# Optimization experiments

Measured on AMD Instinct MI355X. Metric: run time of the kernel, lower is better.

Reference implementation:

```python
import math
import jax, jax.numpy as jnp
import numpy as np

B, N, CS, CZ, CH, H, PQ, PV = 1, 4096, 512, 128, 64, 16, 4, 8
BQ, BK = 32, 128
NB = N // BQ
CZ4 = CZ // 4
INF = 100000.0
EPS = 1e-8


def quat_to_rot(q):
    w, x, y, z = q[..., 0], q[..., 1], q[..., 2], q[..., 3]
    return jnp.stack([
        jnp.stack([1 - 2 * (y * y + z * z), 2 * (x * y - w * z), 2 * (x * z + w * y)], -1),
        jnp.stack([2 * (x * y + w * z), 1 - 2 * (x * x + z * z), 2 * (y * z - w * x)], -1),
        jnp.stack([2 * (x * z - w * y), 2 * (y * z + w * x), 1 - 2 * (x * x + y * y)], -1),
    ], -2)


def setup_inputs() -> dict:
    key = jax.random.key(0)
    ks = jax.random.split(key, 16)
    s = jax.random.normal(ks[0], (B, N, CS), jnp.float32)
    z = jax.random.normal(ks[1], (B, NB, BQ, BK, CZ), jnp.float32)
    trans = jax.random.normal(ks[2], (B, N, 3), jnp.float32) * 10.0
    quat = jax.random.normal(ks[3], (B, N, 4), jnp.float32)
    quat = quat / jnp.linalg.norm(quat, axis=-1, keepdims=True)
    rots = quat_to_rot(quat)
    s_mask = jnp.ones((B, N), jnp.float32)
    pad = (BK - BQ) // 2  # key window centered on each query block
    key_idx = (jnp.arange(NB)[:, None] * BQ - pad + jnp.arange(BK)[None, :]).astype(jnp.int32)

    def w(k, shp):
        return jax.random.normal(k, shp, jnp.float32) * (1.0 / math.sqrt(shp[0]))

    return {
        's': s, 'z': z, 'trans': trans, 'rots': rots, 's_mask': s_mask, 'key_idx': key_idx,
        'Wq': w(ks[4], (CS, H * CH)), 'Wk': w(ks[5], (CS, H * CH)), 'Wv': w(ks[6], (CS, H * CH)),
        'Wqp': w(ks[7], (CS, H * PQ * 3)), 'Wkvp': w(ks[8], (CS, H * (PQ + PV) * 3)),
        'Wb': w(ks[9], (CZ, H)), 'Wdz': w(ks[10], (CZ, CZ4)),
        'head_weights': jnp.full((H,), float(np.log(np.e - 1.0)), jnp.float32),  # softplus^-1(1)
        'Wout': w(ks[11], (H * (CZ4 + CH + PV * 4), CS)),
        'g_s': jnp.ones((CS,), jnp.float32), 'b_s': jnp.zeros((CS,), jnp.float32),
        'g_z': jnp.ones((CZ,), jnp.float32), 'b_z': jnp.zeros((CZ,), jnp.float32),
    }


def _ln(x, g, b):
    m = jnp.mean(x, -1, keepdims=True)
    v = jnp.mean((x - m) ** 2, -1, keepdims=True)
    return (x - m) * jax.lax.rsqrt(v + 1e-5) * g + b


def _ipa(s, z, trans, rots, s_mask, key_idx, Wq, Wk, Wv, Wqp, Wkvp, Wb, Wdz,
         head_weights, Wout, g_s, b_s, g_z, b_z):
    s_n = _ln(s, g_s, b_s)
    z_n = _ln(z, g_z, b_z)

    valid = (key_idx >= 0) & (key_idx < N)            # [NB, BK]
    idx = jnp.clip(key_idx, 0, N - 1)
    vf = valid.astype(s.dtype)[None]                  # [1, NB, BK]

    def gk(x):  # gather key window: [B,N,...] -> [B,NB,BK,...]
        return x[:, idx]

    sq = s_n.reshape(B, NB, BQ, CS)
    sk = gk(s_n) * vf[..., None]                      # zero-pad out-of-range keys

    tq = trans.reshape(B, NB, BQ, 3)
    rq = rots.reshape(B, NB, BQ, 3, 3)
    tk = gk(trans) * vf[..., None]
    rk = jnp.where(valid[None, :, :, None, None], gk(rots), jnp.eye(3, dtype=rots.dtype))

    q = (sq @ Wq).reshape(B, NB, BQ, H, CH)
    k = (sk @ Wk).reshape(B, NB, BK, H, CH)
    v = (sk @ Wv).reshape(B, NB, BK, H, CH)

    q_pts = (sq @ Wqp).reshape(B, NB, BQ, H * PQ, 3)
    q_pts = jnp.einsum('bnqij,bnqpj->bnqpi', rq, q_pts) + tq[:, :, :, None, :]
    q_pts = q_pts.reshape(B, NB, BQ, H, PQ, 3)

    kv_pts = (sk @ Wkvp).reshape(B, NB, BK, H * (PQ + PV), 3)
    kv_pts = jnp.einsum('bnkij,bnkpj->bnkpi', rk, kv_pts) + tk[:, :, :, None, :]
    kv_pts = kv_pts.reshape(B, NB, BK, H, PQ + PV, 3)
    k_pts, v_pts = kv_pts[..., :PQ, :], kv_pts[..., PQ:, :]

    bias = jnp.einsum('bnqkc,ch->bnqkh', z_n, Wb)
    a = jnp.einsum('bnqhc,bnkhc->bnqkh', q, k) * math.sqrt(1.0 / (3 * CH))
    a = a + math.sqrt(1.0 / 3) * bias

    disp = q_pts[:, :, :, None] - k_pts[:, :, None]   # [B,NB,BQ,BK,H,PQ,3]
    pt_att = jnp.sum(disp ** 2, -1)                   # [B,NB,BQ,BK,H,PQ]
    hw = jax.nn.softplus(head_weights) * math.sqrt(1.0 / (3 * (PQ * 9.0 / 2)))
    pt_att = -0.5 * jnp.sum(pt_att * hw[:, None], -1)  # [B,NB,BQ,BK,H]

    qm = s_mask.reshape(B, NB, BQ)
    km = gk(s_mask) * vf
    amask = INF * (qm[:, :, :, None] * km[:, :, None, :] - 1.0)

    a = a + pt_att + amask[..., None]
    a = jax.nn.softmax(jnp.swapaxes(a, -1, -2), axis=-1)  # [B,NB,BQ,H,BK]

    o = jnp.einsum('bnqhk,bnkhc->bnqhc', a, v).reshape(B, NB, BQ, H * CH)

    o_pt = jnp.einsum('bnqhk,bnkhpc->bnqhpc', a, v_pts)
    o_pt = jnp.einsum('bnqji,bnqhpj->bnqhpi', rq, o_pt - tq[:, :, :, None, None, :])
    o_pt_norm = jnp.sqrt(jnp.sum(o_pt ** 2, -1) + EPS).reshape(B, NB, BQ, H * PV)
    o_pt = o_pt.reshape(B, NB, BQ, H * PV * 3)

    pair_z = z_n @ Wdz                                # [B,NB,BQ,BK,CZ4]
    o_pair = jnp.einsum('bnqhk,bnqkc->bnqhc', a, pair_z).reshape(B, NB, BQ, H * CZ4)

    out = jnp.concatenate([o, o_pt, o_pt_norm, o_pair], -1) @ Wout
    return out.reshape(B, N, CS)


def reference(s, z, trans, rots, s_mask, key_idx, Wq, Wk, Wv, Wqp, Wkvp, Wb, Wdz,
              head_weights, Wout, g_s, b_s, g_z, b_z):
    return _ipa(s, z, trans, rots, s_mask, key_idx, Wq, Wk, Wv, Wqp, Wkvp, Wb, Wdz,
                head_weights, Wout, g_s, b_s, g_z, b_z)
```

## Files before the change

### kernel.cpp

```cpp
#include <hip/hip_runtime.h>
#include <math.h>

#define D_N 4096
#define PBW 3072
#define PPW 768
#define OFFK 1024
#define OFFV 2048
#define CATW 2048

typedef __bf16 bf16_t;
typedef __bf16 bf16x8 __attribute__((ext_vector_type(8)));
typedef __bf16 bf16x4 __attribute__((ext_vector_type(4)));
typedef float f32x4 __attribute__((ext_vector_type(4)));

__device__ __forceinline__ void gld16(const void* g, void* l) {
    __builtin_amdgcn_global_load_lds((const __attribute__((address_space(1))) unsigned int*)g,
                                     (__attribute__((address_space(3))) unsigned int*)l, 16, 0, 0);
}

__global__ __launch_bounds__(256) void k_prep(
    const float* __restrict__ Wq, const float* __restrict__ Wk, const float* __restrict__ Wv,
    const float* __restrict__ Wqp, const float* __restrict__ Wkvp, const float* __restrict__ Wout,
    const float* __restrict__ Wb, const float* __restrict__ Wdz,
    const float* __restrict__ gz, const float* __restrict__ bz,
    const float* __restrict__ s, const float* __restrict__ g_s, const float* __restrict__ b_s,
    bf16_t* __restrict__ wcatT, bf16_t* __restrict__ WoutT,
    bf16_t* __restrict__ WzT, float* __restrict__ Kv, bf16_t* __restrict__ s_nb)
{
    __shared__ float T[64][65];
    const int bx = blockIdx.x;
    const int tid = threadIdx.x;
    if (bx < 736) {
        const float* src; int ld, coff, r0;
        bf16_t* dst; int Rdst;
        if (bx < 480) {
            int c0 = (bx % 60) * 64;
            r0 = (bx / 60) * 64;
            if (c0 < 1024)      { src = Wq;   ld = 1024; coff = c0; }
            else if (c0 < 2048) { src = Wk;   ld = 1024; coff = c0 - 1024; }
            else if (c0 < 3072) { src = Wv;   ld = 1024; coff = c0 - 2048; }
            else if (c0 < 3264) { src = Wqp;  ld = 192;  coff = c0 - 3072; }
            else                { src = Wkvp; ld = 576;  coff = c0 - 3264; }
            dst = wcatT + (size_t)c0 * 512; Rdst = 512;
        } else {
            int b = bx - 480;
            int c0 = (b & 7) * 64;
            r0 = (b >> 3) * 64;
            src = Wout; ld = 512; coff = c0;
            dst = WoutT + (size_t)c0 * 2048; Rdst = 2048;
        }
        {
            int rr = tid >> 2, cb = (tid & 3) * 16;
            const float* p = src + (size_t)(r0 + rr) * ld + coff + cb;
            #pragma unroll
            for (int i = 0; i < 4; ++i)
                *(float4*)&T[rr][cb + i * 4] = *(const float4*)(p + i * 4);
        }
        __syncthreads();
        {
            int cc = tid >> 2, rb = (tid & 3) * 16;
            bf16_t* o = dst + (size_t)cc * Rdst + r0 + rb;
            bf16x8 o0, o1;
            #pragma unroll
            for (int j = 0; j < 8; ++j) o0[j] = (bf16_t)T[rb + j][cc];
            #pragma unroll
            for (int j = 0; j < 8; ++j) o1[j] = (bf16_t)T[rb + 8 + j][cc];
            *(bf16x8*)(o) = o0;
            *(bf16x8*)(o + 8) = o1;
        }
    } else if (bx == 736) {
        for (int i = tid; i < 6144; i += 256) {
            int j = i >> 7, c = i & 127;
            float w = (j < 16) ? Wb[c * 16 + j] : Wdz[c * 32 + (j - 16)];
            WzT[i] = (bf16_t)(gz[c] * w);
        }
        if (tid < 48) {
            int j = tid;
            float acc = 0.f;
            for (int c = 0; c < 128; ++c) {
                float w = (j < 16) ? Wb[c * 16 + j] : Wdz[c * 32 + (j - 16)];
                acc += bz[c] * w;
            }
            Kv[j] = acc;
        }
    } else {
        int row = (bx - 737) * 4 + (tid >> 6);
        int lane = tid & 63;
        const float4* p = (const float4*)(s + (size_t)row * 512);
        float4 v0 = p[lane];
        float4 v1 = p[lane + 64];
        float sum = v0.x + v0.y + v0.z + v0.w + v1.x + v1.y + v1.z + v1.w;
        float sq  = v0.x*v0.x + v0.y*v0.y + v0.z*v0.z + v0.w*v0.w
                  + v1.x*v1.x + v1.y*v1.y + v1.z*v1.z + v1.w*v1.w;
        #pragma unroll
        for (int off = 1; off < 64; off <<= 1) {
            sum += __shfl_xor(sum, off);
            sq  += __shfl_xor(sq, off);
        }
        float m = sum * (1.0f / 512.0f);
        float var = sq * (1.0f / 512.0f) - m * m;
        float rs = rsqrtf(var + 1e-5f);
        int c = lane * 4;
        int c2 = 256 + lane * 4;
        bf16x4 r0, r1;
        r0[0] = (bf16_t)((v0.x - m) * rs * g_s[c+0] + b_s[c+0]);
        r0[1] = (bf16_t)((v0.y - m) * rs * g_s[c+1] + b_s[c+1]);
        r0[2] = (bf16_t)((v0.z - m) * rs * g_s[c+2] + b_s[c+2]);
        r0[3] = (bf16_t)((v0.w - m) * rs * g_s[c+3] + b_s[c+3]);
        r1[0] = (bf16_t)((v1.x - m) * rs * g_s[c2+0] + b_s[c2+0]);
        r1[1] = (bf16_t)((v1.y - m) * rs * g_s[c2+1] + b_s[c2+1]);
        r1[2] = (bf16_t)((v1.z - m) * rs * g_s[c2+2] + b_s[c2+2]);
        r1[3] = (bf16_t)((v1.w - m) * rs * g_s[c2+3] + b_s[c2+3]);
        *(bf16x4*)(s_nb + (size_t)row * 512 + c)  = r0;
        *(bf16x4*)(s_nb + (size_t)row * 512 + c2) = r1;
    }
}

__global__ __launch_bounds__(256) void gemm_proj(const bf16_t* __restrict__ A, const bf16_t* __restrict__ BT,
    bf16_t* __restrict__ projb, float* __restrict__ projp)
{
    __shared__ bf16_t Asl[128][32];
    __shared__ bf16_t Bsl[128][32];
    const int tid = threadIdx.x, lane = tid & 63, w = tid >> 6;
    const int row0 = blockIdx.y * 128, col0 = blockIdx.x * 128;
    const int wr = (w >> 1) * 64, wc = (w & 1) * 64;
    const int K = 512;
    const int sr = lane >> 2, k8 = (lane & 3) * 8;
    const bf16_t* Ab = A + (size_t)(row0 + w * 32 + sr) * K + k8;
    const bf16_t* Bb = BT + (size_t)(col0 + w * 32 + sr) * K + k8;
    f32x4 acc[4][4];
    #pragma unroll
    for (int m = 0; m < 4; ++m)
        #pragma unroll
        for (int n = 0; n < 4; ++n) acc[m][n] = (f32x4){0.f,0.f,0.f,0.f};
    for (int k0 = 0; k0 < K; k0 += 32) {
        __syncthreads();
        gld16(Ab + k0,          &Asl[w * 32][0]);
        gld16(Ab + k0 + 16 * K, &Asl[w * 32 + 16][0]);
        gld16(Bb + k0,          &Bsl[w * 32][0]);
        gld16(Bb + k0 + 16 * K, &Bsl[w * 32 + 16][0]);
        __syncthreads();
        bf16x8 af[4], bfr[4];
        #pragma unroll
        for (int m = 0; m < 4; ++m) af[m]  = *(const bf16x8*)&Asl[wr + m*16 + (lane & 15)][(lane >> 4) * 8];
        #pragma unroll
        for (int n = 0; n < 4; ++n) bfr[n] = *(const bf16x8*)&Bsl[wc + n*16 + (lane & 15)][(lane >> 4) * 8];
        #pragma unroll
        for (int m = 0; m < 4; ++m)
            #pragma unroll
            for (int n = 0; n < 4; ++n)
                acc[m][n] = __builtin_amdgcn_mfma_f32_16x16x32_bf16(af[m], bfr[n], acc[m][n], 0, 0, 0);
    }
    if (col0 < 3072) {
        #pragma unroll
        for (int m = 0; m < 4; ++m)
            #pragma unroll
            for (int n = 0; n < 4; ++n)
                #pragma unroll
                for (int i = 0; i < 4; ++i)
                    projb[(size_t)(row0 + wr + m*16 + (lane >> 4)*4 + i) * PBW + col0 + wc + n*16 + (lane & 15)]
                        = (bf16_t)acc[m][n][i];
    } else {
        #pragma unroll
        for (int m = 0; m < 4; ++m)
            #pragma unroll
            for (int n = 0; n < 4; ++n)
                #pragma unroll
                for (int i = 0; i < 4; ++i)
                    projp[(size_t)(row0 + wr + m*16 + (lane >> 4)*4 + i) * PPW + col0 - 3072 + wc + n*16 + (lane & 15)]
                        = acc[m][n][i];
    }
}

__global__ __launch_bounds__(256) void k_zbias4(const float* __restrict__ z,
    const bf16_t* __restrict__ WzT, const float* __restrict__ Kv,
    float* __restrict__ biasT, bf16_t* __restrict__ pzT)
{
    __shared__ __align__(16) float zbuf[2][64][128];
    const int tid = threadIdx.x, lane = tid & 63, w = tid >> 6;
    const int r16 = lane & 15, kg = lane >> 4;
    bf16x8 bfz[3][4];
    #pragma unroll
    for (int nt = 0; nt < 3; ++nt)
        #pragma unroll
        for (int kc = 0; kc < 4; ++kc)
            bfz[nt][kc] = *(const bf16x8*)(WzT + (size_t)(nt * 16 + r16) * 128 + kc * 32 + kg * 8);
    float K0 = Kv[r16], K1 = Kv[16 + r16], K2 = Kv[32 + r16];
    asm volatile("s_waitcnt vmcnt(0)" ::: "memory");
    __builtin_amdgcn_sched_barrier(0);

    const int gid = blockIdx.x * 4 + w;
    const char* zb = (const char*)z + (size_t)gid * 64 * 512;
    char* lb0 = (char*)&zbuf[0][w * 16][0];
    char* lb1 = (char*)&zbuf[1][w * 16][0];

#define STAGE(i, lb) { \
    const char* gp_ = zb + (size_t)(i) * 8192 + lane * 16; \
    _Pragma("unroll") \
    for (int c_ = 0; c_ < 8; ++c_) gld16(gp_ + c_ * 1024, (lb) + c_ * 1024); }

#define PROCESS(i, b) { \
    const float* rp = &zbuf[b][w * 16 + r16][kg * 8]; \
    float4 za[4], zc[4]; \
    float sum = 0.f, sq = 0.f; \
    _Pragma("unroll") \
    for (int kc = 0; kc < 4; ++kc) { \
        float4 a_ = *(const float4*)(rp + kc * 32); \
        float4 b_ = *(const float4*)(rp + kc * 32 + 4); \
        za[kc] = a_; zc[kc] = b_; \
        sum += a_.x + a_.y + a_.z + a_.w + b_.x + b_.y + b_.z + b_.w; \
        sq  += a_.x*a_.x + a_.y*a_.y + a_.z*a_.z + a_.w*a_.w + b_.x*b_.x + b_.y*b_.y + b_.z*b_.z + b_.w*b_.w; \
    } \
    sum += __shfl_xor(sum, 16); sq += __shfl_xor(sq, 16); \
    sum += __shfl_xor(sum, 32); sq += __shfl_xor(sq, 32); \
    float m_ = sum * (1.0f / 128.0f); \
    float rs_ = rsqrtf(sq * (1.0f / 128.0f) - m_ * m_ + 1e-5f); \
    bf16x8 af[4]; \
    _Pragma("unroll") \
    for (int kc = 0; kc < 4; ++kc) { \
        af[kc][0] = (bf16_t)((za[kc].x - m_) * rs_); \
        af[kc][1] = (bf16_t)((za[kc].y - m_) * rs_); \
        af[kc][2] = (bf16_t)((za[kc].z - m_) * rs_); \
        af[kc][3] = (bf16_t)((za[kc].w - m_) * rs_); \
        af[kc][4] = (bf16_t)((zc[kc].x - m_) * rs_); \
        af[kc][5] = (bf16_t)((zc[kc].y - m_) * rs_); \
        af[kc][6] = (bf16_t)((zc[kc].z - m_) * rs_); \
        af[kc][7] = (bf16_t)((zc[kc].w - m_) * rs_); \
    } \
    f32x4 acc0 = (f32x4){0.f,0.f,0.f,0.f}; \
    f32x4 acc1 = (f32x4){0.f,0.f,0.f,0.f}; \
    f32x4 acc2 = (f32x4){0.f,0.f,0.f,0.f}; \
    _Pragma("unroll") \
    for (int kc = 0; kc < 4; ++kc) { \
        acc0 = __builtin_amdgcn_mfma_f32_16x16x32_bf16(af[kc], bfz[0][kc], acc0, 0, 0, 0); \
        acc1 = __builtin_amdgcn_mfma_f32_16x16x32_bf16(af[kc], bfz[1][kc], acc1, 0, 0, 0); \
        acc2 = __builtin_amdgcn_mfma_f32_16x16x32_bf16(af[kc], bfz[2][kc], acc2, 0, 0, 0); \
    } \
    const int t_ = gid * 4 + (i); \
    const int rowq_ = t_ >> 3; \
    const int k0_ = ((t_ & 7) << 4) + kg * 4; \
    float4 bw = {acc0[0] + K0, acc0[1] + K0, acc0[2] + K0, acc0[3] + K0}; \
    *(float4*)&biasT[((size_t)rowq_ * 16 + r16) * 128 + k0_] = bw; \
    bf16x4 p1, p2; \
    _Pragma("unroll") \
    for (int i2 = 0; i2 < 4; ++i2) { p1[i2] = (bf16_t)(acc1[i2] + K1); p2[i2] = (bf16_t)(acc2[i2] + K2); } \
    *(bf16x4*)&pzT[((size_t)rowq_ * 32 + r16) * 128 + k0_] = p1; \
    *(bf16x4*)&pzT[((size_t)rowq_ * 32 + 16 + r16) * 128 + k0_] = p2; }

#define LDS_DRAIN asm volatile("s_waitcnt lgkmcnt(0)" ::: "memory"); __builtin_amdgcn_sched_barrier(0);

    STAGE(0, lb0);
    STAGE(1, lb1);
    asm volatile("s_waitcnt vmcnt(8)" ::: "memory");
    __builtin_amdgcn_sched_barrier(0);
    PROCESS(0, 0);
    LDS_DRAIN
    STAGE(2, lb0);
    asm volatile("s_waitcnt vmcnt(8)" ::: "memory");
    __builtin_amdgcn_sched_barrier(0);
    PROCESS(1, 1);
    LDS_DRAIN
    STAGE(3, lb1);
    asm volatile("s_waitcnt vmcnt(8)" ::: "memory");
    __builtin_amdgcn_sched_barrier(0);
    PROCESS(2, 0);
    asm volatile("s_waitcnt vmcnt(0)" ::: "memory");
    __builtin_amdgcn_sched_barrier(0);
    PROCESS(3, 1);
#undef STAGE
#undef PROCESS
#undef LDS_DRAIN
}

__global__ __launch_bounds__(256) void k_attn4(
    const bf16_t* __restrict__ projb, const float* __restrict__ projp,
    const float* __restrict__ biasT, const float* __restrict__ rots,
    const float* __restrict__ trans, const float* __restrict__ smask,
    const int* __restrict__ kidx, const float* __restrict__ hwraw,
    bf16_t* __restrict__ catb, bf16_t* __restrict__ Pbf)
{
    __shared__ __align__(16) char pool[51840];
    bf16_t (*Qs)[72]   = (bf16_t(*)[72])pool;
    bf16_t (*Ks)[72]   = (bf16_t(*)[72])(pool + 32 * 72 * 2);
    bf16_t (*Vt)[136]  = (bf16_t(*)[136])pool;
    float  (*att)[132] = (float(*)[132])(pool + 26112);
    bf16_t (*Ps)[136]  = (bf16_t(*)[136])(pool + 26112);
    float  (*optmp)[33]= (float(*)[33])(pool + 26112 + 8704);
    float  (*kp_s)[12] = (float(*)[12])(pool + 43008);
    float  (*qp_s)[12] = (float(*)[12])(pool + 49152);
    float*  km_s       = (float*)(pool + 50688);
    float*  qm_s       = (float*)(pool + 51200);
    int*    rows_s     = (int*)(pool + 51328);

    const int wgid = blockIdx.x;
    const int swz = (wgid & 7) * 256 + (wgid >> 3);
    const int h = swz >> 7;
    const int nblk = swz & 127;
    const int tid = threadIdx.x;
    const int lane = tid & 63;
    const int w = tid >> 6;
    const int rowq0 = nblk * 32;
    const float hw = log1pf(__expf(hwraw[h])) * 0.13608276348795434f;

    if (tid < 128) {
        int ki = kidx[nblk * 128 + tid];
        int valid = (ki >= 0 && ki < D_N);
        int rr = ki < 0 ? 0 : (ki > D_N - 1 ? D_N - 1 : ki);
        rows_s[tid] = rr;
        km_s[tid] = valid ? smask[rr] : 0.0f;
    } else if (tid < 160) {
        qm_s[tid - 128] = smask[rowq0 + tid - 128];
    }
    __syncthreads();
    {
        int q = tid >> 3, cg = (tid & 7) * 8;
        *(bf16x8*)&Qs[q][cg] = *(const bf16x8*)(projb + (size_t)(rowq0 + q) * PBW + h * 64 + cg);
    }
    float Rk[9], tk0 = 0.f, tk1 = 0.f, tk2 = 0.f;
    if (tid < 128) {
        int rr = rows_s[tid];
        const float* Rp = rots + (size_t)rr * 9;
        const float* tp = trans + (size_t)rr * 3;
        #pragma unroll
        for (int e = 0; e < 9; ++e) Rk[e] = Rp[e];
        tk0 = tp[0]; tk1 = tp[1]; tk2 = tp[2];
        const float* kp = projp + (size_t)rr * PPW + 192 + h * 36;
        float4 p0 = *(const float4*)kp;
        float4 p1 = *(const float4*)(kp + 4);
        float4 p2 = *(const float4*)(kp + 8);
        float xs[4] = {p0.x, p0.w, p1.z, p2.y};
        float ys[4] = {p0.y, p1.x, p1.w, p2.z};
        float zs[4] = {p0.z, p1.y, p2.x, p2.w};
        #pragma unroll
        for (int p = 0; p < 4; ++p) {
            kp_s[tid][p*3+0] = Rk[0]*xs[p] + Rk[1]*ys[p] + Rk[2]*zs[p] + tk0;
            kp_s[tid][p*3+1] = Rk[3]*xs[p] + Rk[4]*ys[p] + Rk[5]*zs[p] + tk1;
            kp_s[tid][p*3+2] = Rk[6]*xs[p] + Rk[7]*ys[p] + Rk[8]*zs[p] + tk2;
        }
    } else {
        int j = tid - 128;
        {
            int q = j >> 2, p = j & 3;
            const float* Rp = rots + (size_t)(rowq0 + q) * 9;
            const float* tp = trans + (size_t)(rowq0 + q) * 3;
            const float* qp = projp + (size_t)(rowq0 + q) * PPW + h * 12 + p * 3;
            float x = qp[0], y = qp[1], zc = qp[2];
            qp_s[q][p*3+0] = Rp[0]*x + Rp[1]*y + Rp[2]*zc + tp[0];
            qp_s[q][p*3+1] = Rp[3]*x + Rp[4]*y + Rp[5]*zc + tp[1];
            qp_s[q][p*3+2] = Rp[6]*x + Rp[7]*y + Rp[8]*zc + tp[2];
        }
        {
            const bf16_t* pK = projb + (size_t)rows_s[j] * PBW + OFFK + h * 64;
            #pragma unroll
            for (int u = 0; u < 8; ++u)
                *(bf16x8*)&Ks[j][u * 8] = *(const bf16x8*)(pK + u * 8);
        }
    }
    __syncthreads();
    {
        #pragma unroll
        for (int j = 0; j < 4; ++j) {
            int T = w * 4 + j;
            int m = T & 1, n = T >> 1;
            f32x4 acc = (f32x4){0.f,0.f,0.f,0.f};
            #pragma unroll
            for (int kc = 0; kc < 2; ++kc) {
                bf16x8 a = *(const bf16x8*)&Qs[m*16 + (lane & 15)][kc*32 + (lane >> 4) * 8];
                bf16x8 b = *(const bf16x8*)&Ks[n*16 + (lane & 15)][kc*32 + (lane >> 4) * 8];
                acc = __builtin_amdgcn_mfma_f32_16x16x32_bf16(a, b, acc, 0, 0, 0);
            }
            #pragma unroll
            for (int i = 0; i < 4; ++i)
                att[m*16 + (lane >> 4)*4 + i][n*16 + (lane & 15)] = acc[i];
        }
    }
    __syncthreads();
    if (tid < 128) {
        const float* vp = projp + (size_t)rows_s[tid] * PPW + 192 + h * 36 + 12;
        float4 a0 = *(const float4*)(vp);
        float4 a1 = *(const float4*)(vp + 4);
        float4 a2 = *(const float4*)(vp + 8);
        float4 a3 = *(const float4*)(vp + 12);
        float4 a4 = *(const float4*)(vp + 16);
        float4 a5 = *(const float4*)(vp + 20);
        float xs[8] = {a0.x, a0.w, a1.z, a2.y, a3.x, a3.w, a4.z, a5.y};
        float ys[8] = {a0.y, a1.x, a1.w, a2.z, a3.y, a4.x, a4.w, a5.z};
        float zs[8] = {a0.z, a1.y, a2.x, a2.w, a3.z, a4.y, a5.x, a5.w};
        #pragma unroll
        for (int p = 0; p < 8; ++p) {
            Vt[64 + p*3 + 0][tid] = (bf16_t)(Rk[0]*xs[p] + Rk[1]*ys[p] + Rk[2]*zs[p] + tk0);
            Vt[64 + p*3 + 1][tid] = (bf16_t)(Rk[3]*xs[p] + Rk[4]*ys[p] + Rk[5]*zs[p] + tk1);
            Vt[64 + p*3 + 2][tid] = (bf16_t)(Rk[6]*xs[p] + Rk[7]*ys[p] + Rk[8]*zs[p] + tk2);
        }
        {
            bf16x8 zz = {};
            *(bf16x8*)&Vt[88 + (tid & 7)][(tid >> 3) * 8] = zz;
        }
    } else {
        int krow = tid - 128;
        const bf16_t* p = projb + (size_t)rows_s[krow] * PBW + OFFV + h * 64;
        #pragma unroll
        for (int u4 = 0; u4 < 8; ++u4) {
            bf16x8 v = *(const bf16x8*)(p + u4 * 8);
            #pragma unroll
            for (int jj = 0; jj < 8; ++jj) Vt[u4 * 8 + jj][krow] = v[jj];
        }
    }
    {
        int q = tid >> 3, kg = tid & 7;
        float qp[12];
        #pragma unroll
        for (int e = 0; e < 12; ++e) qp[e] = qp_s[q][e];
        float qm = qm_s[q];
        const float* bT = biasT + ((size_t)(rowq0 + q) * 16 + h) * 128;
        #pragma unroll
        for (int j2 = 0; j2 < 16; ++j2) {
            int k = kg + j2 * 8;
            float4 k0 = *(const float4*)&kp_s[k][0];
            float4 k1 = *(const float4*)&kp_s[k][4];
            float4 k2 = *(const float4*)&kp_s[k][8];
            float d0 = qp[0]-k0.x, d1 = qp[1]-k0.y, d2_ = qp[2]-k0.z, d3 = qp[3]-k0.w;
            float d4 = qp[4]-k1.x, d5 = qp[5]-k1.y, d6 = qp[6]-k1.z, d7 = qp[7]-k1.w;
            float d8 = qp[8]-k2.x, d9 = qp[9]-k2.y, d10 = qp[10]-k2.z, d11 = qp[11]-k2.w;
            float dd = d0*d0+d1*d1+d2_*d2_+d3*d3+d4*d4+d5*d5+d6*d6+d7*d7+d8*d8+d9*d9+d10*d10+d11*d11;
            float val = att[q][k] * 0.07216878364870323f
                      + 0.5773502691896258f * bT[k]
                      + 100000.0f * (qm * km_s[k] - 1.0f)
                      - 0.5f * hw * dd;
            att[q][k] = val;
        }
    }
    __syncthreads();
    {
        int q = tid >> 3, kg = tid & 7;
        float l[16];
        #pragma unroll
        for (int j2 = 0; j2 < 16; ++j2) l[j2] = att[q][kg + j2 * 8];
        float mx = l[0];
        #pragma unroll
        for (int j2 = 1; j2 < 16; ++j2) mx = fmaxf(mx, l[j2]);
        mx = fmaxf(mx, __shfl_xor(mx, 1));
        mx = fmaxf(mx, __shfl_xor(mx, 2));
        mx = fmaxf(mx, __shfl_xor(mx, 4));
        float se = 0.f;
        #pragma unroll
        for (int j2 = 0; j2 < 16; ++j2) { l[j2] = __expf(l[j2] - mx); se += l[j2]; }
        se += __shfl_xor(se, 1);
        se += __shfl_xor(se, 2);
        se += __shfl_xor(se, 4);
        float inv = 1.0f / se;
        __syncthreads();
        bf16_t* pg = Pbf + ((size_t)(rowq0 + q) * 16 + h) * 128;
        #pragma unroll
        for (int j2 = 0; j2 < 16; ++j2) {
            bf16_t pb = (bf16_t)(l[j2] * inv);
            Ps[q][kg + j2 * 8] = pb;
            pg[kg + j2 * 8] = pb;
        }
    }
    __syncthreads();
    {
        #pragma unroll
        for (int j = 0; j < 3; ++j) {
            int T = w * 3 + j;
            int m = T & 1, n = T >> 1;
            f32x4 acc = (f32x4){0.f,0.f,0.f,0.f};
            #pragma unroll
            for (int kc = 0; kc < 4; ++kc) {
                bf16x8 a = *(const bf16x8*)&Ps[m*16 + (lane & 15)][kc*32 + (lane >> 4) * 8];
                bf16x8 b = *(const bf16x8*)&Vt[n*16 + (lane & 15)][kc*32 + (lane >> 4) * 8];
                acc = __builtin_amdgcn_mfma_f32_16x16x32_bf16(a, b, acc, 0, 0, 0);
            }
            int rowb = m * 16 + (lane >> 4) * 4;
            int col = lane & 15;
            if (n < 4) {
                #pragma unroll
                for (int i = 0; i < 4; ++i)
                    catb[(size_t)(rowq0 + rowb + i) * CATW + h * 64 + n * 16 + col] = (bf16_t)acc[i];
            } else {
                #pragma unroll
                for (int i = 0; i < 4; ++i)
                    optmp[rowb + i][(n - 4) * 16 + col] = acc[i];
            }
        }
    }
    __syncthreads();
    {
        int q = tid >> 3, pp = tid & 7;
        float sx = optmp[q][pp * 3 + 0];
        float sy = optmp[q][pp * 3 + 1];
        float sz = optmp[q][pp * 3 + 2];
        const float* R = rots + (size_t)(rowq0 + q) * 9;
        const float* t = trans + (size_t)(rowq0 + q) * 3;
        float x = sx - t[0], y = sy - t[1], z2 = sz - t[2];
        float ox = R[0] * x + R[3] * y + R[6] * z2;
        float oy = R[1] * x + R[4] * y + R[7] * z2;
        float oz = R[2] * x + R[5] * y + R[8] * z2;
        bf16_t* cp = catb + (size_t)(rowq0 + q) * CATW;
        cp[1024 + h * 24 + pp * 3 + 0] = (bf16_t)ox;
        cp[1024 + h * 24 + pp * 3 + 1] = (bf16_t)oy;
        cp[1024 + h * 24 + pp * 3 + 2] = (bf16_t)oz;
        cp[1408 + h * 8 + pp] = (bf16_t)sqrtf(ox * ox + oy * oy + oz * oz + 1e-8f);
    }
}

__global__ __launch_bounds__(256) void k_opair(const bf16_t* __restrict__ Pbf,
    const bf16_t* __restrict__ pzT, bf16_t* __restrict__ catb)
{
    int tid = threadIdx.x, lane = tid & 63, w = tid >> 6;
    size_t rowq = (size_t)blockIdx.x * 4 + w;
    const bf16_t* Pp = Pbf + rowq * 2048;
    const bf16_t* zp = pzT + rowq * 4096;
    bf16x8 pa[4];
    #pragma unroll
    for (int kc = 0; kc < 4; ++kc)
        pa[kc] = *(const bf16x8*)(Pp + (size_t)(lane & 15) * 128 + kc * 32 + (lane >> 4) * 8);
    #pragma unroll
    for (int ct = 0; ct < 2; ++ct) {
        f32x4 acc = (f32x4){0.f,0.f,0.f,0.f};
        #pragma unroll
        for (int kc = 0; kc < 4; ++kc) {
            bf16x8 b = *(const bf16x8*)(zp + (size_t)(ct * 16 + (lane & 15)) * 128 + kc * 32 + (lane >> 4) * 8);
            acc = __builtin_amdgcn_mfma_f32_16x16x32_bf16(pa[kc], b, acc, 0, 0, 0);
        }
        #pragma unroll
        for (int i = 0; i < 4; ++i) {
            int hh = (lane >> 4) * 4 + i;
            catb[rowq * CATW + 1536 + hh * 32 + ct * 16 + (lane & 15)] = (bf16_t)acc[i];
        }
    }
}

__global__ __launch_bounds__(256) void gemm_out(const bf16_t* __restrict__ A, const bf16_t* __restrict__ BT,
    float* __restrict__ C)
{
    __shared__ bf16_t Asl[64][32];
    __shared__ bf16_t Bsl[128][32];
    const int tid = threadIdx.x, lane = tid & 63, w = tid >> 6;
    const int row0 = blockIdx.y * 64, col0 = blockIdx.x * 128;
    const int wr = (w >> 1) * 32, wc = (w & 1) * 64;
    const int K = 2048;
    const int sr = lane >> 2, k8 = (lane & 3) * 8;
    const bf16_t* Ab = A + (size_t)(row0 + w * 16 + sr) * K + k8;
    const bf16_t* Bb = BT + (size_t)(col0 + w * 32 + sr) * K + k8;
    f32x4 acc[2][4];
    #pragma unroll
    for (int m = 0; m < 2; ++m)
        #pragma unroll
        for (int n = 0; n < 4; ++n) acc[m][n] = (f32x4){0.f,0.f,0.f,0.f};
    for (int k0 = 0; k0 < K; k0 += 32) {
        __syncthreads();
        gld16(Ab + k0,          &Asl[w * 16][0]);
        gld16(Bb + k0,          &Bsl[w * 32][0]);
        gld16(Bb + k0 + 16 * K, &Bsl[w * 32 + 16][0]);
        __syncthreads();
        bf16x8 af[2], bfr[4];
        #pragma unroll
        for (int m = 0; m < 2; ++m) af[m]  = *(const bf16x8*)&Asl[wr + m*16 + (lane & 15)][(lane >> 4) * 8];
        #pragma unroll
        for (int n = 0; n < 4; ++n) bfr[n] = *(const bf16x8*)&Bsl[wc + n*16 + (lane & 15)][(lane >> 4) * 8];
        #pragma unroll
        for (int m = 0; m < 2; ++m)
            #pragma unroll
            for (int n = 0; n < 4; ++n)
                acc[m][n] = __builtin_amdgcn_mfma_f32_16x16x32_bf16(af[m], bfr[n], acc[m][n], 0, 0, 0);
    }
    #pragma unroll
    for (int m = 0; m < 2; ++m)
        #pragma unroll
        for (int n = 0; n < 4; ++n)
            #pragma unroll
            for (int i = 0; i < 4; ++i)
                C[(size_t)(row0 + wr + m*16 + (lane >> 4)*4 + i) * 512 + col0 + wc + n*16 + (lane & 15)] = acc[m][n][i];
}

extern "C" void kernel_launch(void* const* d_in, const int* in_sizes, int n_in,
                              void* d_out, int out_size, void* d_ws, size_t ws_size,
                              hipStream_t stream)
{
    (void)in_sizes; (void)n_in; (void)out_size;
    const float* s     = (const float*)d_in[0];
    const float* z     = (const float*)d_in[1];
    const float* trans = (const float*)d_in[2];
    const float* rots  = (const float*)d_in[3];
    const float* smask = (const float*)d_in[4];
    const int*   kidx  = (const int*)d_in[5];
    const float* Wq    = (const float*)d_in[6];
    const float* Wk    = (const float*)d_in[7];
    const float* Wv    = (const float*)d_in[8];
    const float* Wqp   = (const float*)d_in[9];
    const float* Wkvp  = (const float*)d_in[10];
    const float* Wb    = (const float*)d_in[11];
    const float* Wdz   = (const float*)d_in[12];
    const float* hw    = (const float*)d_in[13];
    const float* Wout  = (const float*)d_in[14];
    const float* g_s   = (const float*)d_in[15];
    const float* b_s   = (const float*)d_in[16];
    const float* g_z   = (const float*)d_in[17];
    const float* b_z   = (const float*)d_in[18];

    char* ws = (char*)d_ws;
    bf16_t* projb = (bf16_t*)(ws);
    float*  projp = (float*)(ws + 25165824);
    float*  biasT = (float*)(ws + 37748736);
    bf16_t* wcatT = (bf16_t*)(ws + 71303168);
    bf16_t* s_nb  = (bf16_t*)(ws + 75235328);
    bf16_t* pzT   = (bf16_t*)(ws + 79429632);
    bf16_t* Pbf   = (bf16_t*)(ws + 112984064);
    bf16_t* catb  = (bf16_t*)(ws + 129761280);
    bf16_t* WoutT = (bf16_t*)(ws + 146538496);
    bf16_t* WzT   = (bf16_t*)(ws + 148635648);
    float*  Kv    = (float*)(ws + 148647936);
    if (ws_size < (size_t)148648128) return;
    float* out = (float*)d_out;

    k_prep<<<1761, 256, 0, stream>>>(Wq, Wk, Wv, Wqp, Wkvp, Wout, Wb, Wdz, g_z, b_z,
                                     s, g_s, b_s, wcatT, WoutT, WzT, Kv, s_nb);
    gemm_proj<<<dim3(30, 32), 256, 0, stream>>>(s_nb, wcatT, projb, projp);
    k_zbias4<<<2048, 256, 0, stream>>>(z, WzT, Kv, biasT, pzT);
    k_attn4<<<2048, 256, 0, stream>>>(projb, projp, biasT, rots, trans, smask, kidx, hw, catb, Pbf);
    k_opair<<<1024, 256, 0, stream>>>(Pbf, pzT, catb);
    gemm_out<<<dim3(4, 64), 256, 0, stream>>>(catb, WoutT, out);
}
```

Baseline: 216.7 us.

## Merge projection GEMM and z-bias kernel into one interleaved launch

Combines the independent projection GEMM and the z-bias/pair-projection kernel into one launch. Block indices are interleaved so one in three blocks runs a GEMM tile and the rest run z tiles. The compute-bound GEMM can then overlap with the bandwidth-bound z streaming, and one launch boundary goes away. In exchange, every block reserves the larger 64KB shared buffer, and the GEMM path's register use may lower occupancy for the z path.

```diff
diff --git a/kernel.cpp b/kernel.cpp
--- a/kernel.cpp
+++ b/kernel.cpp
@@ -116,68 +116,79 @@
     }
 }
 
-__global__ __launch_bounds__(256) void gemm_proj(const bf16_t* __restrict__ A, const bf16_t* __restrict__ BT,
-    bf16_t* __restrict__ projb, float* __restrict__ projp)
-{
-    __shared__ bf16_t Asl[128][32];
-    __shared__ bf16_t Bsl[128][32];
-    const int tid = threadIdx.x, lane = tid & 63, w = tid >> 6;
-    const int row0 = blockIdx.y * 128, col0 = blockIdx.x * 128;
-    const int wr = (w >> 1) * 64, wc = (w & 1) * 64;
-    const int K = 512;
-    const int sr = lane >> 2, k8 = (lane & 3) * 8;
-    const bf16_t* Ab = A + (size_t)(row0 + w * 32 + sr) * K + k8;
-    const bf16_t* Bb = BT + (size_t)(col0 + w * 32 + sr) * K + k8;
-    f32x4 acc[4][4];
-    #pragma unroll
-    for (int m = 0; m < 4; ++m)
-        #pragma unroll
-        for (int n = 0; n < 4; ++n) acc[m][n] = (f32x4){0.f,0.f,0.f,0.f};
-    for (int k0 = 0; k0 < K; k0 += 32) {
-        __syncthreads();
-        gld16(Ab + k0,          &Asl[w * 32][0]);
-        gld16(Ab + k0 + 16 * K, &Asl[w * 32 + 16][0]);
-        gld16(Bb + k0,          &Bsl[w * 32][0]);
-        gld16(Bb + k0 + 16 * K, &Bsl[w * 32 + 16][0]);
-        __syncthreads();
-        bf16x8 af[4], bfr[4];
-        #pragma unroll
-        for (int m = 0; m < 4; ++m) af[m]  = *(const bf16x8*)&Asl[wr + m*16 + (lane & 15)][(lane >> 4) * 8];
-        #pragma unroll
-        for (int n = 0; n < 4; ++n) bfr[n] = *(const bf16x8*)&Bsl[wc + n*16 + (lane & 15)][(lane >> 4) * 8];
-        #pragma unroll
-        for (int m = 0; m < 4; ++m)
-            #pragma unroll
-            for (int n = 0; n < 4; ++n)
-                acc[m][n] = __builtin_amdgcn_mfma_f32_16x16x32_bf16(af[m], bfr[n], acc[m][n], 0, 0, 0);
-    }
-    if (col0 < 3072) {
-        #pragma unroll
-        for (int m = 0; m < 4; ++m)
-            #pragma unroll
-            for (int n = 0; n < 4; ++n)
-                #pragma unroll
-                for (int i = 0; i < 4; ++i)
-                    projb[(size_t)(row0 + wr + m*16 + (lane >> 4)*4 + i) * PBW + col0 + wc + n*16 + (lane & 15)]
-                        = (bf16_t)acc[m][n][i];
-    } else {
-        #pragma unroll
-        for (int m = 0; m < 4; ++m)
-            #pragma unroll
-            for (int n = 0; n < 4; ++n)
-                #pragma unroll
-                for (int i = 0; i < 4; ++i)
-                    projp[(size_t)(row0 + wr + m*16 + (lane >> 4)*4 + i) * PPW + col0 - 3072 + wc + n*16 + (lane & 15)]
-                        = acc[m][n][i];
-    }
-}
-
-__global__ __launch_bounds__(256) void k_zbias4(const float* __restrict__ z,
-    const bf16_t* __restrict__ WzT, const float* __restrict__ Kv,
+__global__ __launch_bounds__(256) void k_fused(
+    const bf16_t* __restrict__ A, const bf16_t* __restrict__ BT,
+    bf16_t* __restrict__ projb, float* __restrict__ projp,
+    const float* __restrict__ z, const bf16_t* __restrict__ WzT, const float* __restrict__ Kv,
     float* __restrict__ biasT, bf16_t* __restrict__ pzT)
 {
-    __shared__ __align__(16) float zbuf[2][64][128];
+    __shared__ __align__(16) char smem[65536];
+    const int bx = blockIdx.x;
     const int tid = threadIdx.x, lane = tid & 63, w = tid >> 6;
+    int gemm_id = -1, zid = 0;
+    if (bx < 2880) {
+        int s3 = bx % 3, b3 = bx / 3;
+        if (s3 == 0) gemm_id = b3;
+        else         zid = b3 * 2 + s3 - 1;
+    } else {
+        zid = 1920 + (bx - 2880);
+    }
+
+    if (gemm_id >= 0) {
+        bf16_t (*Asl)[32] = (bf16_t(*)[32])smem;
+        bf16_t (*Bsl)[32] = (bf16_t(*)[32])(smem + 8192);
+        const int row0 = (gemm_id / 30) * 128, col0 = (gemm_id % 30) * 128;
+        const int wr = (w >> 1) * 64, wc = (w & 1) * 64;
+        const int K = 512;
+        const int sr = lane >> 2, k8 = (lane & 3) * 8;
+        const bf16_t* Ab = A + (size_t)(row0 + w * 32 + sr) * K + k8;
+        const bf16_t* Bb = BT + (size_t)(col0 + w * 32 + sr) * K + k8;
+        f32x4 acc[4][4];
+        #pragma unroll
+        for (int m = 0; m < 4; ++m)
+            #pragma unroll
+            for (int n = 0; n < 4; ++n) acc[m][n] = (f32x4){0.f,0.f,0.f,0.f};
+        for (int k0 = 0; k0 < K; k0 += 32) {
+            __syncthreads();
+            gld16(Ab + k0,          &Asl[w * 32][0]);
+            gld16(Ab + k0 + 16 * K, &Asl[w * 32 + 16][0]);
+            gld16(Bb + k0,          &Bsl[w * 32][0]);
+            gld16(Bb + k0 + 16 * K, &Bsl[w * 32 + 16][0]);
+            __syncthreads();
+            bf16x8 af[4], bfr[4];
+            #pragma unroll
+            for (int m = 0; m < 4; ++m) af[m]  = *(const bf16x8*)&Asl[wr + m*16 + (lane & 15)][(lane >> 4) * 8];
+            #pragma unroll
+            for (int n = 0; n < 4; ++n) bfr[n] = *(const bf16x8*)&Bsl[wc + n*16 + (lane & 15)][(lane >> 4) * 8];
+            #pragma unroll
+            for (int m = 0; m < 4; ++m)
+                #pragma unroll
+                for (int n = 0; n < 4; ++n)
+                    acc[m][n] = __builtin_amdgcn_mfma_f32_16x16x32_bf16(af[m], bfr[n], acc[m][n], 0, 0, 0);
+        }
+        if (col0 < 3072) {
+            #pragma unroll
+            for (int m = 0; m < 4; ++m)
+                #pragma unroll
+                for (int n = 0; n < 4; ++n)
+                    #pragma unroll
+                    for (int i = 0; i < 4; ++i)
+                        projb[(size_t)(row0 + wr + m*16 + (lane >> 4)*4 + i) * PBW + col0 + wc + n*16 + (lane & 15)]
+                            = (bf16_t)acc[m][n][i];
+        } else {
+            #pragma unroll
+            for (int m = 0; m < 4; ++m)
+                #pragma unroll
+                for (int n = 0; n < 4; ++n)
+                    #pragma unroll
+                    for (int i = 0; i < 4; ++i)
+                        projp[(size_t)(row0 + wr + m*16 + (lane >> 4)*4 + i) * PPW + col0 - 3072 + wc + n*16 + (lane & 15)]
+                            = acc[m][n][i];
+        }
+        return;
+    }
+
+    float (*zbuf)[64][128] = (float(*)[64][128])smem;
     const int r16 = lane & 15, kg = lane >> 4;
     bf16x8 bfz[3][4];
     #pragma unroll
@@ -189,7 +200,7 @@
     asm volatile("s_waitcnt vmcnt(0)" ::: "memory");
     __builtin_amdgcn_sched_barrier(0);
 
-    const int gid = blockIdx.x * 4 + w;
+    const int gid = zid * 4 + w;
     const char* zb = (const char*)z + (size_t)gid * 64 * 512;
     char* lb0 = (char*)&zbuf[0][w * 16][0];
     char* lb1 = (char*)&zbuf[1][w * 16][0];
@@ -616,8 +627,7 @@
 
     k_prep<<<1761, 256, 0, stream>>>(Wq, Wk, Wv, Wqp, Wkvp, Wout, Wb, Wdz, g_z, b_z,
                                      s, g_s, b_s, wcatT, WoutT, WzT, Kv, s_nb);
-    gemm_proj<<<dim3(30, 32), 256, 0, stream>>>(s_nb, wcatT, projb, projp);
-    k_zbias4<<<2048, 256, 0, stream>>>(z, WzT, Kv, biasT, pzT);
+    k_fused<<<3008, 256, 0, stream>>>(s_nb, wcatT, projb, projp, z, WzT, Kv, biasT, pzT);
     k_attn4<<<2048, 256, 0, stream>>>(projb, projp, biasT, rots, trans, smask, kidx, hw, catb, Pbf);
     k_opair<<<1024, 256, 0, stream>>>(Pbf, pzT, catb);
     gemm_out<<<dim3(4, 64), 256, 0, stream>>>(catb, WoutT, out);
```

After: 222.6 us. +2.7%, slower.
